# Kernel tuning notes

Measured on AMD Instinct MI355X. Metric: run time of the kernel, lower is better.

## Reference

```python
import jax, jax.numpy as jnp
import numpy as np

N = 50000      # nodes
E = 500000     # edges (avg degree 10)
D_IN = 256     # input feature dim
HID = 256      # hidden_channels
HEADS = 8
C_HID = HID // HEADS   # 32 per-head dim for concat layers
NCLS = 8               # num_classes (last layer per-head dim, concat=False)


def setup_inputs() -> dict:
    key = jax.random.key(0)
    keys = iter(jax.random.split(key, 64))
    def w(shape, s=0.05):
        return jax.random.normal(next(keys), shape, jnp.float32) * s
    inp = {}
    inp["x"] = jax.random.normal(next(keys), (N, D_IN), jnp.float32)
    inp["edge_index"] = jax.random.randint(next(keys), (2, E), 0, N, jnp.int32)
    # (fan_in, heads*per_head_out, skip_out) per layer; layer3: concat=False
    layer_cfg = [(D_IN, HEADS * C_HID, HEADS * C_HID),
                 (HID, HEADS * C_HID, HEADS * C_HID),
                 (HID, HEADS * NCLS, NCLS)]
    for i, (fin, hc, skip) in enumerate(layer_cfg, 1):
        for nm in ("q", "k", "v"):
            inp[f"W{nm}{i}"] = w((fin, hc))
            inp[f"b{nm}{i}"] = jnp.zeros((hc,), jnp.float32)
        inp[f"Ws{i}"] = w((fin, skip))
        inp[f"bs{i}"] = jnp.zeros((skip,), jnp.float32)
        inp[f"Wb{i}"] = w((3 * skip, 1))
    for i in (1, 2):
        inp[f"ln{i}_g"] = jnp.ones((HID,), jnp.float32)
        inp[f"ln{i}_b"] = jnp.zeros((HID,), jnp.float32)
    return inp


def _layer_norm(x, g, b):
    mu = x.mean(-1, keepdims=True)
    var = ((x - mu) ** 2).mean(-1, keepdims=True)
    return (x - mu) * jax.lax.rsqrt(var + 1e-5) * g + b


def _tconv(x, src, dst, Wq, bq, Wk, bk, Wv, bv, Ws, bs, Wb, concat):
    """PyG TransformerConv with beta=True, root_weight=True, eval-mode (no dropout)."""
    n = x.shape[0]
    q = (x @ Wq + bq).reshape(n, HEADS, -1)   # [N,H,C]
    k = (x @ Wk + bk).reshape(n, HEADS, -1)
    v = (x @ Wv + bv).reshape(n, HEADS, -1)
    C = q.shape[-1]
    # per-edge attention logits, scaled dot product
    logits = (q[dst] * k[src]).sum(-1) * jax.lax.rsqrt(jnp.float32(C))  # [E,H]
    # segment softmax over incoming edges of each dst node
    m = jax.ops.segment_max(logits, dst, num_segments=n)                # [N,H]
    m = jnp.where(jnp.isfinite(m), m, 0.0)                              # empty segments
    e = jnp.exp(logits - m[dst])
    s = jax.ops.segment_sum(e, dst, num_segments=n)
    alpha = e / (s[dst] + 1e-16)                                        # [E,H]
    # scatter-aggregate messages
    out = jax.ops.segment_sum(v[src] * alpha[:, :, None], dst, num_segments=n)  # [N,H,C]
    out = out.reshape(n, -1) if concat else out.mean(axis=1)
    # beta-gated skip connection
    xr = x @ Ws + bs
    beta = jax.nn.sigmoid(jnp.concatenate([out, xr, out - xr], axis=-1) @ Wb)   # [N,1]
    return beta * xr + (1.0 - beta) * out


def reference(x, edge_index,
              Wq1, bq1, Wk1, bk1, Wv1, bv1, Ws1, bs1, Wb1,
              Wq2, bq2, Wk2, bk2, Wv2, bv2, Ws2, bs2, Wb2,
              Wq3, bq3, Wk3, bk3, Wv3, bv3, Ws3, bs3, Wb3,
              ln1_g, ln1_b, ln2_g, ln2_b):
    src, dst = edge_index[0], edge_index[1]
    h = jax.nn.relu(_layer_norm(
        _tconv(x, src, dst, Wq1, bq1, Wk1, bk1, Wv1, bv1, Ws1, bs1, Wb1, True),
        ln1_g, ln1_b))
    h = jax.nn.relu(_layer_norm(
        _tconv(h, src, dst, Wq2, bq2, Wk2, bk2, Wv2, bv2, Ws2, bs2, Wb2, True),
        ln2_g, ln2_b))
    return _tconv(h, src, dst, Wq3, bq3, Wk3, bk3, Wv3, bv3, Ws3, bs3, Wb3, False)
```

## Files before the change

kernel.cpp:

```cpp
#include <hip/hip_runtime.h>
#include <stdint.h>

typedef __attribute__((ext_vector_type(8))) short short8;
typedef __attribute__((ext_vector_type(4))) float f32x4;

struct us4 { unsigned short x, y, z, w; };

__device__ __forceinline__ float b2f(unsigned short u){
  union { unsigned int i; float f; } x; x.i = ((unsigned int)u) << 16; return x.f;
}
__device__ __forceinline__ unsigned short f2b(float f){
  union { float f; unsigned int i; } x; x.f = f;
  unsigned int i = x.i;
  unsigned int r = (i + 0x7FFFu + ((i >> 16) & 1u)) >> 16;
  return (unsigned short)r;
}
__device__ __forceinline__ float sane(float v){
  return fminf(fmaxf(v, -1e30f), 1e30f);
}
__device__ __forceinline__ float lclamp(float v){
  return fminf(fmaxf(v, -60.f), 60.f);
}
__device__ __forceinline__ float ldin(const void* p, size_t i, int f32){
  return f32 ? ((const float*)p)[i] : b2f(((const unsigned short*)p)[i]);
}

__global__ void k_flag(const unsigned short* __restrict__ xu, int* __restrict__ flag){
  __shared__ int cnt;
  if (threadIdx.x == 0) cnt = 0;
  __syncthreads();
  unsigned u = xu[2 * threadIdx.x];
  int e = (u >> 7) & 0xFF;
  if (e >= 97 && e <= 132) atomicAdd(&cnt, 1);
  __syncthreads();
  if (threadIdx.x == 0) flag[0] = (cnt >= 192) ? 0 : 1;
}

__global__ void k_cvt(const void* __restrict__ xin, unsigned short* __restrict__ xb,
                      int n4, const int* __restrict__ flagp){
  int f32 = *flagp;
  int i = blockIdx.x * 256 + threadIdx.x;
  if (i < n4){
    if (f32){
      float4 v = ((const float4*)xin)[i];
      us4 o = { f2b(v.x), f2b(v.y), f2b(v.z), f2b(v.w) };
      ((us4*)xb)[i] = o;
    } else {
      ((us4*)xb)[i] = ((const us4*)xin)[i];
    }
  }
}

__global__ void k_deg(const int* __restrict__ ei, int E, int N, int* __restrict__ deg){
  int e = blockIdx.x * 256 + threadIdx.x;
  if (e < E){
    unsigned d = (unsigned)ei[E + e];
    if (d < (unsigned)N) atomicAdd(&deg[d], 1);
  }
}

__global__ void k_bsum(const int* __restrict__ deg, int N, int* __restrict__ bsum){
  int b = blockIdx.x, t = threadIdx.x;
  int i0 = b * 1024 + t * 4;
  int s = 0;
  if (i0 + 4 <= N){
    int4 v = *(const int4*)&deg[i0];
    s = v.x + v.y + v.z + v.w;
  } else {
    #pragma unroll
    for (int j = 0; j < 4; ++j){ int i = i0 + j; if (i < N) s += deg[i]; }
  }
  #pragma unroll
  for (int off = 32; off; off >>= 1) s += __shfl_xor(s, off);
  __shared__ int ws[4];
  if ((t & 63) == 0) ws[t >> 6] = s;
  __syncthreads();
  if (t == 0) bsum[b] = ws[0] + ws[1] + ws[2] + ws[3];
}

__global__ void k_bscan(const int* __restrict__ bsum, int nb,
                        int* __restrict__ boff, int* __restrict__ rowptr, int N){
  int t = threadIdx.x;
  if (nb <= 64){
    int v = (t < nb) ? bsum[t] : 0;
    int inc = v;
    #pragma unroll
    for (int off = 1; off < 64; off <<= 1){
      int u = __shfl_up(inc, off);
      if (t >= off) inc += u;
    }
    if (t < nb) boff[t] = inc - v;
    if (t == 63) rowptr[N] = inc;
  } else {
    if (t == 0){
      int run = 0;
      for (int i = 0; i < nb; ++i){ boff[i] = run; run += bsum[i]; }
      rowptr[N] = run;
    }
  }
}

__global__ void k_rowptr(const int* __restrict__ deg, const int* __restrict__ boff,
                         int N, int* __restrict__ rowptr, int* __restrict__ cursor){
  int b = blockIdx.x, t = threadIdx.x;
  int i0 = b * 1024 + t * 4;
  int d0 = 0, d1 = 0, d2 = 0, d3 = 0;
  if (i0 + 4 <= N){
    int4 v = *(const int4*)&deg[i0];
    d0 = v.x; d1 = v.y; d2 = v.z; d3 = v.w;
  } else {
    if (i0     < N) d0 = deg[i0];
    if (i0 + 1 < N) d1 = deg[i0 + 1];
    if (i0 + 2 < N) d2 = deg[i0 + 2];
    if (i0 + 3 < N) d3 = deg[i0 + 3];
  }
  int s = d0 + d1 + d2 + d3;
  int lane = t & 63, w = t >> 6;
  int inc = s;
  #pragma unroll
  for (int off = 1; off < 64; off <<= 1){
    int u = __shfl_up(inc, off);
    if (lane >= off) inc += u;
  }
  int wex = inc - s;
  __shared__ int wtot[4];
  if (lane == 63) wtot[w] = inc;
  __syncthreads();
  int cross = 0;
  for (int i = 0; i < w; ++i) cross += wtot[i];
  int basev = boff[b] + cross + wex;
  int r0 = basev, r1 = basev + d0, r2 = r1 + d1, r3 = r2 + d2;
  if (i0 + 4 <= N){
    int4 o = { r0, r1, r2, r3 };
    *(int4*)&rowptr[i0] = o;
    *(int4*)&cursor[i0] = o;
  } else {
    if (i0     < N){ rowptr[i0]   = r0; cursor[i0]   = r0; }
    if (i0 + 1 < N){ rowptr[i0+1] = r1; cursor[i0+1] = r1; }
    if (i0 + 2 < N){ rowptr[i0+2] = r2; cursor[i0+2] = r2; }
    if (i0 + 3 < N){ rowptr[i0+3] = r3; cursor[i0+3] = r3; }
  }
}

__global__ void k_scatter(const int* __restrict__ ei, int E, int N,
                          int* __restrict__ cursor, int* __restrict__ srcs){
  int e = blockIdx.x * 256 + threadIdx.x;
  if (e < E){
    unsigned d = (unsigned)ei[E + e];
    if (d < (unsigned)N){
      int pos = atomicAdd(&cursor[d], 1);
      if ((unsigned)pos < (unsigned)E){
        unsigned s = (unsigned)ei[e];
        srcs[pos] = (s < (unsigned)N) ? (int)s : 0;
      }
    }
  }
}

__global__ void k_pack(const void* __restrict__ Wq, const void* __restrict__ bq,
                       const void* __restrict__ Wk, const void* __restrict__ bk,
                       const void* __restrict__ Wv, const void* __restrict__ bv,
                       const void* __restrict__ Ws, const void* __restrict__ bs,
                       unsigned short* __restrict__ WT, float* __restrict__ bias,
                       int Mq, int Ms, int K, const int* __restrict__ flagp){
  int f32 = *flagp;
  int cg = blockIdx.x;
  int k  = threadIdx.x;
  int mat, c, mc;
  if (cg < 3 * Mq){ mat = cg / Mq; c = cg % Mq; mc = Mq; }
  else if (cg < 3 * Mq + Ms){ mat = 3; c = cg - 3 * Mq; mc = Ms; }
  else { mat = 4; c = 0; mc = 1; }
  const void* W = (mat==0)?Wq:(mat==1)?Wk:(mat==2)?Wv:(mat==3)?Ws:(const void*)0;
  WT[(size_t)cg * K + k] = (mat < 4) ? f2b(ldin(W, (size_t)k * mc + c, f32)) : (unsigned short)0;
  if (k == 0){
    const void* B = (mat==0)?bq:(mat==1)?bk:(mat==2)?bv:(mat==3)?bs:(const void*)0;
    bias[cg] = (mat < 4) ? ldin(B, c, f32) : 0.f;
  }
}

__global__ __launch_bounds__(256) void k_gemm(const unsigned short* __restrict__ A,
                                              const unsigned short* __restrict__ WT,
                                              const float* __restrict__ bias,
                                              unsigned short* __restrict__ B0,
                                              unsigned short* __restrict__ B1,
                                              unsigned short* __restrict__ B2,
                                              unsigned short* __restrict__ B3,
                                              int N, int Mout, int secshift){
  __shared__ __align__(16) unsigned short Alds[64][264];
  __shared__ __align__(16) unsigned short Clds[32][276];
  int tid = threadIdx.x, wid = tid >> 6, lane = tid & 63;
  int l15 = lane & 15, l4 = lane >> 4;
  int row0 = blockIdx.x * 64;
  {
    int srow = tid >> 2, sc4 = tid & 3;
    int ar = row0 + srow; if (ar >= N) ar = N - 1;
    const unsigned short* Ap = A + (size_t)ar * 256;
    #pragma unroll
    for (int i = 0; i < 8; ++i){
      int col = (sc4 + 4 * i) * 8;
      *(short8*)&Alds[srow][col] = *(const short8*)&Ap[col];
    }
  }
  __syncthreads();
  int secw = 1 << secshift;
  int strow = tid >> 3, stchunk = tid & 7;
  for (int cb = wid * 64; cb < Mout; cb += 256){
    f32x4 acc[4][4] = {};
    #pragma unroll
    for (int k0 = 0; k0 < 256; k0 += 32){
      short8 a0 = *(const short8*)&Alds[l15     ][k0 + l4*8];
      short8 a1 = *(const short8*)&Alds[16 + l15][k0 + l4*8];
      short8 a2 = *(const short8*)&Alds[32 + l15][k0 + l4*8];
      short8 a3 = *(const short8*)&Alds[48 + l15][k0 + l4*8];
      const unsigned short* wb = WT + (size_t)(cb + l15) * 256 + k0 + l4*8;
      short8 b0 = *(const short8*)(wb);
      short8 b1 = *(const short8*)(wb + 16*256);
      short8 b2 = *(const short8*)(wb + 32*256);
      short8 b3 = *(const short8*)(wb + 48*256);
      acc[0][0] = __builtin_amdgcn_mfma_f32_16x16x32_bf16(a0, b0, acc[0][0], 0,0,0);
      acc[0][1] = __builtin_amdgcn_mfma_f32_16x16x32_bf16(a0, b1, acc[0][1], 0,0,0);
      acc[0][2] = __builtin_amdgcn_mfma_f32_16x16x32_bf16(a0, b2, acc[0][2], 0,0,0);
      acc[0][3] = __builtin_amdgcn_mfma_f32_16x16x32_bf16(a0, b3, acc[0][3], 0,0,0);
      acc[1][0] = __builtin_amdgcn_mfma_f32_16x16x32_bf16(a1, b0, acc[1][0], 0,0,0);
      acc[1][1] = __builtin_amdgcn_mfma_f32_16x16x32_bf16(a1, b1, acc[1][1], 0,0,0);
      acc[1][2] = __builtin_amdgcn_mfma_f32_16x16x32_bf16(a1, b2, acc[1][2], 0,0,0);
      acc[1][3] = __builtin_amdgcn_mfma_f32_16x16x32_bf16(a1, b3, acc[1][3], 0,0,0);
      acc[2][0] = __builtin_amdgcn_mfma_f32_16x16x32_bf16(a2, b0, acc[2][0], 0,0,0);
      acc[2][1] = __builtin_amdgcn_mfma_f32_16x16x32_bf16(a2, b1, acc[2][1], 0,0,0);
      acc[2][2] = __builtin_amdgcn_mfma_f32_16x16x32_bf16(a2, b2, acc[2][2], 0,0,0);
      acc[2][3] = __builtin_amdgcn_mfma_f32_16x16x32_bf16(a2, b3, acc[2][3], 0,0,0);
      acc[3][0] = __builtin_amdgcn_mfma_f32_16x16x32_bf16(a3, b0, acc[3][0], 0,0,0);
      acc[3][1] = __builtin_amdgcn_mfma_f32_16x16x32_bf16(a3, b1, acc[3][1], 0,0,0);
      acc[3][2] = __builtin_amdgcn_mfma_f32_16x16x32_bf16(a3, b2, acc[3][2], 0,0,0);
      acc[3][3] = __builtin_amdgcn_mfma_f32_16x16x32_bf16(a3, b3, acc[3][3], 0,0,0);
    }
    int gb = cb - wid * 64;
    #pragma unroll
    for (int ph = 0; ph < 2; ++ph){
      #pragma unroll
      for (int rt2 = 0; rt2 < 2; ++rt2){
        int rt = ph*2 + rt2;
        #pragma unroll
        for (int ct = 0; ct < 4; ++ct){
          float bv = bias[cb + ct*16 + l15];
          #pragma unroll
          for (int r = 0; r < 4; ++r)
            Clds[rt2*16 + l4*4 + r][wid*64 + ct*16 + l15] = f2b(acc[rt][ct][r] + bv);
        }
      }
      __syncthreads();
      int grow = row0 + ph*32 + strow;
      if (grow < N){
        int g0 = gb + stchunk * 32;
        int mat = g0 >> secshift;
        int cc  = g0 & (secw - 1);
        unsigned short* Bp = (mat==0)?B0:(mat==1)?B1:(mat==2)?B2:B3;
        unsigned short* dst = Bp + (size_t)grow * secw + cc;
        const unsigned short* srcp = &Clds[strow][stchunk * 32];
        #pragma unroll
        for (int j = 0; j < 4; ++j)
          *(short8*)(dst + j*8) = *(const short8*)(srcp + j*8);
      }
      __syncthreads();
    }
  }
}

__global__ __launch_bounds__(256) void k_attn(const unsigned short* __restrict__ qb,
                                              const unsigned short* __restrict__ kb,
                                              const unsigned short* __restrict__ vb,
                                              const unsigned short* __restrict__ xb,
                                              const int* __restrict__ rowptr,
                                              const int* __restrict__ srcs,
                                              const void* __restrict__ Wb,
                                              const void* __restrict__ lng,
                                              const void* __restrict__ lnb,
                                              unsigned short* __restrict__ hout,
                                              int N, int E, const int* __restrict__ flagp){
  int f32 = *flagp;
  int tid = threadIdx.x, w = tid >> 6, l = tid & 63;
  int n = blockIdx.x * 4 + w;
  if (n >= N) return;
  size_t base = (size_t)n * 256;
  us4 qv = *(const us4*)&qb[base + l*4];
  float q0 = b2f(qv.x), q1 = b2f(qv.y), q2 = b2f(qv.z), q3 = b2f(qv.w);
  int e0 = rowptr[n], e1 = rowptr[n+1];
  if (e0 < 0) e0 = 0;
  if (e1 > E) e1 = E;
  const float scale = 0.17677669529663687f;
  float ss = 0.f, o0 = 0.f, o1 = 0.f, o2 = 0.f, o3 = 0.f;
  int e = e0;
  for (; e + 4 <= e1; e += 4){
    unsigned s0 = (unsigned)srcs[e];   if (s0 >= (unsigned)N) s0 = 0;
    unsigned s1 = (unsigned)srcs[e+1]; if (s1 >= (unsigned)N) s1 = 0;
    unsigned s2 = (unsigned)srcs[e+2]; if (s2 >= (unsigned)N) s2 = 0;
    unsigned s3 = (unsigned)srcs[e+3]; if (s3 >= (unsigned)N) s3 = 0;
    us4 kA = *(const us4*)&kb[(size_t)s0*256 + l*4];
    us4 kB = *(const us4*)&kb[(size_t)s1*256 + l*4];
    us4 kC = *(const us4*)&kb[(size_t)s2*256 + l*4];
    us4 kD = *(const us4*)&kb[(size_t)s3*256 + l*4];
    us4 vA = *(const us4*)&vb[(size_t)s0*256 + l*4];
    us4 vB = *(const us4*)&vb[(size_t)s1*256 + l*4];
    us4 vC = *(const us4*)&vb[(size_t)s2*256 + l*4];
    us4 vD = *(const us4*)&vb[(size_t)s3*256 + l*4];
    float pa = q0*b2f(kA.x) + q1*b2f(kA.y) + q2*b2f(kA.z) + q3*b2f(kA.w);
    float pb = q0*b2f(kB.x) + q1*b2f(kB.y) + q2*b2f(kB.z) + q3*b2f(kB.w);
    float pc = q0*b2f(kC.x) + q1*b2f(kC.y) + q2*b2f(kC.z) + q3*b2f(kC.w);
    float pd = q0*b2f(kD.x) + q1*b2f(kD.y) + q2*b2f(kD.z) + q3*b2f(kD.w);
    pa += __shfl_xor(pa, 1); pa += __shfl_xor(pa, 2); pa += __shfl_xor(pa, 4);
    pb += __shfl_xor(pb, 1); pb += __shfl_xor(pb, 2); pb += __shfl_xor(pb, 4);
    pc += __shfl_xor(pc, 1); pc += __shfl_xor(pc, 2); pc += __shfl_xor(pc, 4);
    pd += __shfl_xor(pd, 1); pd += __shfl_xor(pd, 2); pd += __shfl_xor(pd, 4);
    float ea = __expf(lclamp(pa * scale));
    float eb = __expf(lclamp(pb * scale));
    float ec = __expf(lclamp(pc * scale));
    float ed = __expf(lclamp(pd * scale));
    ss += ea + eb + ec + ed;
    o0 += ea*b2f(vA.x) + eb*b2f(vB.x) + ec*b2f(vC.x) + ed*b2f(vD.x);
    o1 += ea*b2f(vA.y) + eb*b2f(vB.y) + ec*b2f(vC.y) + ed*b2f(vD.y);
    o2 += ea*b2f(vA.z) + eb*b2f(vB.z) + ec*b2f(vC.z) + ed*b2f(vD.z);
    o3 += ea*b2f(vA.w) + eb*b2f(vB.w) + ec*b2f(vC.w) + ed*b2f(vD.w);
  }
  for (; e < e1; ++e){
    unsigned s = (unsigned)srcs[e]; if (s >= (unsigned)N) s = 0;
    us4 kk = *(const us4*)&kb[(size_t)s*256 + l*4];
    us4 vv = *(const us4*)&vb[(size_t)s*256 + l*4];
    float p = q0*b2f(kk.x) + q1*b2f(kk.y) + q2*b2f(kk.z) + q3*b2f(kk.w);
    p += __shfl_xor(p, 1); p += __shfl_xor(p, 2); p += __shfl_xor(p, 4);
    float a = __expf(lclamp(p * scale));
    ss += a;
    o0 += a*b2f(vv.x); o1 += a*b2f(vv.y); o2 += a*b2f(vv.z); o3 += a*b2f(vv.w);
  }
  float sinv = 1.f / (ss + 1e-16f);
  o0 = sane(o0 * sinv); o1 = sane(o1 * sinv);
  o2 = sane(o2 * sinv); o3 = sane(o3 * sinv);
  int c = l * 4;
  us4 xv = *(const us4*)&xb[base + c];
  float x0 = sane(b2f(xv.x)), x1 = sane(b2f(xv.y)), x2 = sane(b2f(xv.z)), x3 = sane(b2f(xv.w));
  float d = o0*ldin(Wb, c+0, f32) + x0*ldin(Wb, 256+c+0, f32) + (o0-x0)*ldin(Wb, 512+c+0, f32)
          + o1*ldin(Wb, c+1, f32) + x1*ldin(Wb, 256+c+1, f32) + (o1-x1)*ldin(Wb, 512+c+1, f32)
          + o2*ldin(Wb, c+2, f32) + x2*ldin(Wb, 256+c+2, f32) + (o2-x2)*ldin(Wb, 512+c+2, f32)
          + o3*ldin(Wb, c+3, f32) + x3*ldin(Wb, 256+c+3, f32) + (o3-x3)*ldin(Wb, 512+c+3, f32);
  #pragma unroll
  for (int off = 32; off; off >>= 1) d += __shfl_xor(d, off);
  float beta = 1.f / (1.f + __expf(-d));
  float r0 = beta*x0 + (1.f-beta)*o0;
  float r1 = beta*x1 + (1.f-beta)*o1;
  float r2 = beta*x2 + (1.f-beta)*o2;
  float r3 = beta*x3 + (1.f-beta)*o3;
  float sm = r0 + r1 + r2 + r3;
  #pragma unroll
  for (int off = 32; off; off >>= 1) sm += __shfl_xor(sm, off);
  float mu = sm * (1.f/256.f);
  float d0 = r0-mu, d1 = r1-mu, d2 = r2-mu, d3 = r3-mu;
  float vv2 = d0*d0 + d1*d1 + d2*d2 + d3*d3;
  #pragma unroll
  for (int off = 32; off; off >>= 1) vv2 += __shfl_xor(vv2, off);
  float rs = rsqrtf(vv2 * (1.f/256.f) + 1e-5f);
  us4 outv;
  outv.x = f2b(fmaxf(d0*rs*ldin(lng,c+0,f32) + ldin(lnb,c+0,f32), 0.f));
  outv.y = f2b(fmaxf(d1*rs*ldin(lng,c+1,f32) + ldin(lnb,c+1,f32), 0.f));
  outv.z = f2b(fmaxf(d2*rs*ldin(lng,c+2,f32) + ldin(lnb,c+2,f32), 0.f));
  outv.w = f2b(fmaxf(d3*rs*ldin(lng,c+3,f32) + ldin(lnb,c+3,f32), 0.f));
  *(us4*)&hout[base + c] = outv;
}

__global__ __launch_bounds__(256) void k_final(const unsigned short* __restrict__ q3,
                                               const unsigned short* __restrict__ k3,
                                               const unsigned short* __restrict__ v3,
                                               const unsigned short* __restrict__ x3,
                                               const int* __restrict__ rowptr,
                                               const int* __restrict__ srcs,
                                               const void* __restrict__ Wb,
                                               void* __restrict__ outp,
                                               int N, int E, const int* __restrict__ flagp){
  int f32 = *flagp;
  int tid = threadIdx.x, w = tid >> 6, l = tid & 63;
  int n = blockIdx.x * 4 + w;
  if (n >= N) return;
  int es = l >> 4, h = (l >> 1) & 7, j = l & 1;
  size_t base = (size_t)n * 64;
  us4 qv = *(const us4*)&q3[base + h*8 + j*4];
  float q0 = b2f(qv.x), q1 = b2f(qv.y), q2 = b2f(qv.z), q3f = b2f(qv.w);
  int e0 = rowptr[n], e1 = rowptr[n+1];
  if (e0 < 0) e0 = 0;
  if (e1 > E) e1 = E;
  int deg = e1 - e0;
  const float scale = 0.35355339059327373f;
  float ss = 0.f, o0 = 0.f, o1 = 0.f, o2 = 0.f, o3 = 0.f;
  for (int ei = es; ei < deg; ei += 4){
    unsigned s = (unsigned)srcs[e0 + ei]; if (s >= (unsigned)N) s = 0;
    us4 kk = *(const us4*)&k3[(size_t)s*64 + h*8 + j*4];
    us4 vv = *(const us4*)&v3[(size_t)s*64 + h*8 + j*4];
    float p = q0*b2f(kk.x) + q1*b2f(kk.y) + q2*b2f(kk.z) + q3f*b2f(kk.w);
    p += __shfl_xor(p, 1);
    float a = __expf(lclamp(p * scale));
    ss += a;
    o0 += a*b2f(vv.x); o1 += a*b2f(vv.y); o2 += a*b2f(vv.z); o3 += a*b2f(vv.w);
  }
  #pragma unroll
  for (int off = 16; off <= 32; off <<= 1){
    ss += __shfl_xor(ss, off);
    o0 += __shfl_xor(o0, off); o1 += __shfl_xor(o1, off);
    o2 += __shfl_xor(o2, off); o3 += __shfl_xor(o3, off);
  }
  float sinv = 1.f / (ss + 1e-16f);
  o0 = sane(o0 * sinv); o1 = sane(o1 * sinv);
  o2 = sane(o2 * sinv); o3 = sane(o3 * sinv);
  #pragma unroll
  for (int off = 2; off <= 8; off <<= 1){
    o0 += __shfl_xor(o0, off); o1 += __shfl_xor(o1, off);
    o2 += __shfl_xor(o2, off); o3 += __shfl_xor(o3, off);
  }
  o0 *= 0.125f; o1 *= 0.125f; o2 *= 0.125f; o3 *= 0.125f;
  us4 xv = *(const us4*)&x3[base + j*4];
  float x0 = sane(b2f(xv.x)), x1 = sane(b2f(xv.y)), x2 = sane(b2f(xv.z)), x3v = sane(b2f(xv.w));
  int c = j*4;
  float d = o0*ldin(Wb, c+0, f32) + x0*ldin(Wb, 8+c+0, f32) + (o0-x0)*ldin(Wb, 16+c+0, f32)
          + o1*ldin(Wb, c+1, f32) + x1*ldin(Wb, 8+c+1, f32) + (o1-x1)*ldin(Wb, 16+c+1, f32)
          + o2*ldin(Wb, c+2, f32) + x2*ldin(Wb, 8+c+2, f32) + (o2-x2)*ldin(Wb, 16+c+2, f32)
          + o3*ldin(Wb, c+3, f32) + x3v*ldin(Wb, 8+c+3, f32) + (o3-x3v)*ldin(Wb, 16+c+3, f32);
  d += __shfl_xor(d, 1);
  float beta = 1.f / (1.f + __expf(-d));
  float r0 = beta*x0  + (1.f-beta)*o0;
  float r1 = beta*x1  + (1.f-beta)*o1;
  float r2 = beta*x2  + (1.f-beta)*o2;
  float r3 = beta*x3v + (1.f-beta)*o3;
  if (l < 2){
    if (f32){
      float* op = (float*)outp + (size_t)n*8 + l*4;
      op[0] = r0; op[1] = r1; op[2] = r2; op[3] = r3;
    } else {
      unsigned short* op = (unsigned short*)outp + (size_t)n*8 + l*4;
      op[0] = f2b(r0); op[1] = f2b(r1); op[2] = f2b(r2); op[3] = f2b(r3);
    }
  }
}

extern "C" void kernel_launch(void* const* d_in, const int* in_sizes, int n_in,
                              void* d_out, int out_size, void* d_ws, size_t ws_size,
                              hipStream_t stream){
  const int* ei = (const int*)d_in[1];
  const int N = in_sizes[0] / 256;
  const int E = in_sizes[1] / 2;

  char* wsp = (char*)d_ws;
  size_t off = 0;
  auto alloc = [&](size_t b) -> void* {
    void* p = wsp + off; off = (off + b + 255) & ~(size_t)255; return p;
  };
  unsigned short* WT1  = (unsigned short*)alloc((size_t)1024*256*2);
  unsigned short* WT2  = (unsigned short*)alloc((size_t)1024*256*2);
  unsigned short* WT3  = (unsigned short*)alloc((size_t)256*256*2);
  float* bias1 = (float*)alloc(1024*4);
  float* bias2 = (float*)alloc(1024*4);
  float* bias3 = (float*)alloc(256*4);
  int* flag   = (int*)alloc(256);
  int* deg    = (int*)alloc((size_t)N*4);
  int* rowptr = (int*)alloc((size_t)(N+1)*4);
  int* cursor = (int*)alloc((size_t)N*4);
  int* bsum   = (int*)alloc(1024*4);
  int* boff   = (int*)alloc(1024*4);
  int* srcs   = (int*)alloc((size_t)E*4);
  unsigned short* xbf = (unsigned short*)alloc((size_t)N*256*2);
  unsigned short* qb  = (unsigned short*)alloc((size_t)N*256*2);
  unsigned short* kb  = (unsigned short*)alloc((size_t)N*256*2);
  unsigned short* vb  = (unsigned short*)alloc((size_t)N*256*2);
  unsigned short* xb  = (unsigned short*)alloc((size_t)N*256*2);
  unsigned short* hbuf= (unsigned short*)alloc((size_t)N*256*2);
  unsigned short* q3 = qb;
  unsigned short* k3 = kb;
  unsigned short* v3 = vb;
  unsigned short* x3 = xb;
  (void)ws_size; (void)n_in; (void)out_size;

  k_flag<<<1, 256, 0, stream>>>((const unsigned short*)d_in[0], flag);
  int n4 = (N * 256) / 4;
  k_cvt<<<(n4 + 255) / 256, 256, 0, stream>>>(d_in[0], xbf, n4, flag);

  hipMemsetAsync(deg, 0, (size_t)N*4, stream);
  int eb = (E + 255) / 256;
  int nbk = (N + 1023) / 1024;
  k_deg<<<eb, 256, 0, stream>>>(ei, E, N, deg);
  k_bsum<<<nbk, 256, 0, stream>>>(deg, N, bsum);
  k_bscan<<<1, 64, 0, stream>>>(bsum, nbk, boff, rowptr, N);
  k_rowptr<<<nbk, 256, 0, stream>>>(deg, boff, N, rowptr, cursor);
  k_scatter<<<eb, 256, 0, stream>>>(ei, E, N, cursor, srcs);

  k_pack<<<1024, 256, 0, stream>>>(d_in[2],  d_in[3],  d_in[4],  d_in[5],  d_in[6],  d_in[7],  d_in[8],  d_in[9],  WT1, bias1, 256, 256, 256, flag);
  k_pack<<<1024, 256, 0, stream>>>(d_in[11], d_in[12], d_in[13], d_in[14], d_in[15], d_in[16], d_in[17], d_in[18], WT2, bias2, 256, 256, 256, flag);
  k_pack<<< 256, 256, 0, stream>>>(d_in[20], d_in[21], d_in[22], d_in[23], d_in[24], d_in[25], d_in[26], d_in[27], WT3, bias3,  64,   8, 256, flag);

  int rb = (N + 63) / 64;
  int nb = (N + 3) / 4;
  k_gemm<<<rb, 256, 0, stream>>>(xbf, WT1, bias1, qb, kb, vb, xb, N, 1024, 8);
  k_attn<<<nb, 256, 0, stream>>>(qb, kb, vb, xb, rowptr, srcs, d_in[10], d_in[29], d_in[30], hbuf, N, E, flag);
  k_gemm<<<rb, 256, 0, stream>>>(hbuf, WT2, bias2, qb, kb, vb, xb, N, 1024, 8);
  k_attn<<<nb, 256, 0, stream>>>(qb, kb, vb, xb, rowptr, srcs, d_in[19], d_in[31], d_in[32], hbuf, N, E, flag);
  k_gemm<<<rb, 256, 0, stream>>>(hbuf, WT3, bias3, q3, k3, v3, x3, N, 256, 6);
  k_final<<<nb, 256, 0, stream>>>(q3, k3, v3, x3, rowptr, srcs, d_in[28], d_out, N, E, flag);
}
```

Baseline: 666.1 us.

## Interleave K/V in fp16, pad CSR rows to 4, prefetch gathers

The GEMM epilogue now writes K and V as fp16 interleaved per 4-channel group, so each edge gather is a single 16-byte load instead of two 8-byte loads. Q and skip outputs also switch to fp16 so the attention dot product can use packed fdot2. CSR rows are padded to multiples of 4 with zeroed slots, and the source indices are pre-multiplied into byte offsets, so the attention loop can read four indices as one vector and software-prefetch the next group with no scalar tail. The cost is fp16 range and precision risk versus bf16, an extra memset of the padded index array, and masked work on the padding slots.

```diff
diff --git a/kernel.cpp b/kernel.cpp
--- a/kernel.cpp
+++ b/kernel.cpp
@@ -3,6 +3,9 @@
 
 typedef __attribute__((ext_vector_type(8))) short short8;
 typedef __attribute__((ext_vector_type(4))) float f32x4;
+typedef __attribute__((ext_vector_type(4))) _Float16 half4;
+typedef __attribute__((ext_vector_type(2))) _Float16 half2v;
+typedef __attribute__((ext_vector_type(4))) int i32x4;
 
 struct us4 { unsigned short x, y, z, w; };
 
@@ -15,6 +18,10 @@
   unsigned int r = (i + 0x7FFFu + ((i >> 16) & 1u)) >> 16;
   return (unsigned short)r;
 }
+__device__ __forceinline__ unsigned short f2h(float f){
+  _Float16 h = (_Float16)f;
+  union { _Float16 h; unsigned short u; } c; c.h = h; return c.u;
+}
 __device__ __forceinline__ float sane(float v){
   return fminf(fmaxf(v, -1e30f), 1e30f);
 }
@@ -23,6 +30,14 @@
 }
 __device__ __forceinline__ float ldin(const void* p, size_t i, int f32){
   return f32 ? ((const float*)p)[i] : b2f(((const unsigned short*)p)[i]);
+}
+__device__ __forceinline__ float dot4h(half2v a0, half2v a1, half2v b0, half2v b1){
+#if __has_builtin(__builtin_amdgcn_fdot2)
+  return __builtin_amdgcn_fdot2(a0, b0, __builtin_amdgcn_fdot2(a1, b1, 0.f, false), false);
+#else
+  return (float)a0.x*(float)b0.x + (float)a0.y*(float)b0.y
+       + (float)a1.x*(float)b1.x + (float)a1.y*(float)b1.y;
+#endif
 }
 
 __global__ void k_flag(const unsigned short* __restrict__ xu, int* __restrict__ flag){
@@ -59,16 +74,18 @@
   }
 }
 
+__device__ __forceinline__ int pad4(int d){ return (d + 3) & ~3; }
+
 __global__ void k_bsum(const int* __restrict__ deg, int N, int* __restrict__ bsum){
   int b = blockIdx.x, t = threadIdx.x;
   int i0 = b * 1024 + t * 4;
   int s = 0;
   if (i0 + 4 <= N){
     int4 v = *(const int4*)&deg[i0];
-    s = v.x + v.y + v.z + v.w;
+    s = pad4(v.x) + pad4(v.y) + pad4(v.z) + pad4(v.w);
   } else {
     #pragma unroll
-    for (int j = 0; j < 4; ++j){ int i = i0 + j; if (i < N) s += deg[i]; }
+    for (int j = 0; j < 4; ++j){ int i = i0 + j; if (i < N) s += pad4(deg[i]); }
   }
   #pragma unroll
   for (int off = 32; off; off >>= 1) s += __shfl_xor(s, off);
@@ -114,7 +131,8 @@
     if (i0 + 2 < N) d2 = deg[i0 + 2];
     if (i0 + 3 < N) d3 = deg[i0 + 3];
   }
-  int s = d0 + d1 + d2 + d3;
+  int p0 = pad4(d0), p1 = pad4(d1), p2 = pad4(d2), p3 = pad4(d3);
+  int s = p0 + p1 + p2 + p3;
   int lane = t & 63, w = t >> 6;
   int inc = s;
   #pragma unroll
@@ -129,7 +147,7 @@
   int cross = 0;
   for (int i = 0; i < w; ++i) cross += wtot[i];
   int basev = boff[b] + cross + wex;
-  int r0 = basev, r1 = basev + d0, r2 = r1 + d1, r3 = r2 + d2;
+  int r0 = basev, r1 = basev + p0, r2 = r1 + p1, r3 = r2 + p2;
   if (i0 + 4 <= N){
     int4 o = { r0, r1, r2, r3 };
     *(int4*)&rowptr[i0] = o;
@@ -142,16 +160,16 @@
   }
 }
 
-__global__ void k_scatter(const int* __restrict__ ei, int E, int N,
+__global__ void k_scatter(const int* __restrict__ ei, int E, int N, int Epad,
                           int* __restrict__ cursor, int* __restrict__ srcs){
   int e = blockIdx.x * 256 + threadIdx.x;
   if (e < E){
     unsigned d = (unsigned)ei[E + e];
     if (d < (unsigned)N){
       int pos = atomicAdd(&cursor[d], 1);
-      if ((unsigned)pos < (unsigned)E){
+      if ((unsigned)pos < (unsigned)Epad){
         unsigned s = (unsigned)ei[e];
-        srcs[pos] = (s < (unsigned)N) ? (int)s : 0;
+        srcs[pos] = (s < (unsigned)N) ? (int)(s * 1024u) : 0;
       }
     }
   }
@@ -181,10 +199,9 @@
 __global__ __launch_bounds__(256) void k_gemm(const unsigned short* __restrict__ A,
                                               const unsigned short* __restrict__ WT,
                                               const float* __restrict__ bias,
-                                              unsigned short* __restrict__ B0,
-                                              unsigned short* __restrict__ B1,
-                                              unsigned short* __restrict__ B2,
-                                              unsigned short* __restrict__ B3,
+                                              unsigned short* __restrict__ qout,
+                                              char* __restrict__ kvout,
+                                              unsigned short* __restrict__ xout,
                                               int N, int Mout, int secshift){
   __shared__ __align__(16) unsigned short Alds[64][264];
   __shared__ __align__(16) unsigned short Clds[32][276];
@@ -245,7 +262,7 @@
           float bv = bias[cb + ct*16 + l15];
           #pragma unroll
           for (int r = 0; r < 4; ++r)
-            Clds[rt2*16 + l4*4 + r][wid*64 + ct*16 + l15] = f2b(acc[rt][ct][r] + bv);
+            Clds[rt2*16 + l4*4 + r][wid*64 + ct*16 + l15] = f2h(acc[rt][ct][r] + bv);
         }
       }
       __syncthreads();
@@ -254,12 +271,21 @@
         int g0 = gb + stchunk * 32;
         int mat = g0 >> secshift;
         int cc  = g0 & (secw - 1);
-        unsigned short* Bp = (mat==0)?B0:(mat==1)?B1:(mat==2)?B2:B3;
-        unsigned short* dst = Bp + (size_t)grow * secw + cc;
         const unsigned short* srcp = &Clds[strow][stchunk * 32];
-        #pragma unroll
-        for (int j = 0; j < 4; ++j)
-          *(short8*)(dst + j*8) = *(const short8*)(srcp + j*8);
+        if (mat == 1 || mat == 2){
+          char* dstb = kvout + (size_t)grow * (size_t)(secw * 4)
+                     + (size_t)((cc >> 2) * 16 + ((mat == 2) ? 8 : 0));
+          #pragma unroll
+          for (int g2 = 0; g2 < 8; ++g2)
+            *(unsigned long long*)(dstb + g2 * 16) =
+                *(const unsigned long long*)(srcp + g2 * 4);
+        } else {
+          unsigned short* Bp = (mat == 0) ? qout : xout;
+          unsigned short* dst = Bp + (size_t)grow * secw + cc;
+          #pragma unroll
+          for (int j = 0; j < 4; ++j)
+            *(short8*)(dst + j*8) = *(const short8*)(srcp + j*8);
+        }
       }
       __syncthreads();
     }
@@ -267,10 +293,10 @@
 }
 
 __global__ __launch_bounds__(256) void k_attn(const unsigned short* __restrict__ qb,
-                                              const unsigned short* __restrict__ kb,
-                                              const unsigned short* __restrict__ vb,
+                                              const char* __restrict__ kvb,
                                               const unsigned short* __restrict__ xb,
                                               const int* __restrict__ rowptr,
+                                              const int* __restrict__ degv,
                                               const int* __restrict__ srcs,
                                               const void* __restrict__ Wb,
                                               const void* __restrict__ lng,
@@ -281,62 +307,60 @@
   int tid = threadIdx.x, w = tid >> 6, l = tid & 63;
   int n = blockIdx.x * 4 + w;
   if (n >= N) return;
-  size_t base = (size_t)n * 256;
-  us4 qv = *(const us4*)&qb[base + l*4];
-  float q0 = b2f(qv.x), q1 = b2f(qv.y), q2 = b2f(qv.z), q3 = b2f(qv.w);
-  int e0 = rowptr[n], e1 = rowptr[n+1];
-  if (e0 < 0) e0 = 0;
-  if (e1 > E) e1 = E;
+  unsigned lof = (unsigned)l * 16u;
+  size_t nbase = (size_t)n * 512;
+  union KV { i32x4 v; _Float16 h[8]; half2v h2[4]; };
+  half4 qv = *(const half4*)((const char*)qb + nbase + (unsigned)l * 8u);
+  half2v q01 = { qv.x, qv.y }, q23 = { qv.z, qv.w };
+  int e0 = rowptr[n]; if (e0 < 0) e0 = 0;
+  int dg = degv[n]; if (dg < 0) dg = 0; if (dg > E) dg = E;
+  int npad = (dg + 3) & ~3;
   const float scale = 0.17677669529663687f;
   float ss = 0.f, o0 = 0.f, o1 = 0.f, o2 = 0.f, o3 = 0.f;
-  int e = e0;
-  for (; e + 4 <= e1; e += 4){
-    unsigned s0 = (unsigned)srcs[e];   if (s0 >= (unsigned)N) s0 = 0;
-    unsigned s1 = (unsigned)srcs[e+1]; if (s1 >= (unsigned)N) s1 = 0;
-    unsigned s2 = (unsigned)srcs[e+2]; if (s2 >= (unsigned)N) s2 = 0;
-    unsigned s3 = (unsigned)srcs[e+3]; if (s3 >= (unsigned)N) s3 = 0;
-    us4 kA = *(const us4*)&kb[(size_t)s0*256 + l*4];
-    us4 kB = *(const us4*)&kb[(size_t)s1*256 + l*4];
-    us4 kC = *(const us4*)&kb[(size_t)s2*256 + l*4];
-    us4 kD = *(const us4*)&kb[(size_t)s3*256 + l*4];
-    us4 vA = *(const us4*)&vb[(size_t)s0*256 + l*4];
-    us4 vB = *(const us4*)&vb[(size_t)s1*256 + l*4];
-    us4 vC = *(const us4*)&vb[(size_t)s2*256 + l*4];
-    us4 vD = *(const us4*)&vb[(size_t)s3*256 + l*4];
-    float pa = q0*b2f(kA.x) + q1*b2f(kA.y) + q2*b2f(kA.z) + q3*b2f(kA.w);
-    float pb = q0*b2f(kB.x) + q1*b2f(kB.y) + q2*b2f(kB.z) + q3*b2f(kB.w);
-    float pc = q0*b2f(kC.x) + q1*b2f(kC.y) + q2*b2f(kC.z) + q3*b2f(kC.w);
-    float pd = q0*b2f(kD.x) + q1*b2f(kD.y) + q2*b2f(kD.z) + q3*b2f(kD.w);
-    pa += __shfl_xor(pa, 1); pa += __shfl_xor(pa, 2); pa += __shfl_xor(pa, 4);
-    pb += __shfl_xor(pb, 1); pb += __shfl_xor(pb, 2); pb += __shfl_xor(pb, 4);
-    pc += __shfl_xor(pc, 1); pc += __shfl_xor(pc, 2); pc += __shfl_xor(pc, 4);
-    pd += __shfl_xor(pd, 1); pd += __shfl_xor(pd, 2); pd += __shfl_xor(pd, 4);
-    float ea = __expf(lclamp(pa * scale));
-    float eb = __expf(lclamp(pb * scale));
-    float ec = __expf(lclamp(pc * scale));
-    float ed = __expf(lclamp(pd * scale));
-    ss += ea + eb + ec + ed;
-    o0 += ea*b2f(vA.x) + eb*b2f(vB.x) + ec*b2f(vC.x) + ed*b2f(vD.x);
-    o1 += ea*b2f(vA.y) + eb*b2f(vB.y) + ec*b2f(vC.y) + ed*b2f(vD.y);
-    o2 += ea*b2f(vA.z) + eb*b2f(vB.z) + ec*b2f(vC.z) + ed*b2f(vD.z);
-    o3 += ea*b2f(vA.w) + eb*b2f(vB.w) + ec*b2f(vC.w) + ed*b2f(vD.w);
-  }
-  for (; e < e1; ++e){
-    unsigned s = (unsigned)srcs[e]; if (s >= (unsigned)N) s = 0;
-    us4 kk = *(const us4*)&kb[(size_t)s*256 + l*4];
-    us4 vv = *(const us4*)&vb[(size_t)s*256 + l*4];
-    float p = q0*b2f(kk.x) + q1*b2f(kk.y) + q2*b2f(kk.z) + q3*b2f(kk.w);
+
+  auto consume = [&](const KV& kv, int valid){
+    float p = dot4h(q01, q23, kv.h2[0], kv.h2[1]);
     p += __shfl_xor(p, 1); p += __shfl_xor(p, 2); p += __shfl_xor(p, 4);
-    float a = __expf(lclamp(p * scale));
+    float a = valid ? __expf(lclamp(p * scale)) : 0.f;
     ss += a;
-    o0 += a*b2f(vv.x); o1 += a*b2f(vv.y); o2 += a*b2f(vv.z); o3 += a*b2f(vv.w);
-  }
+    o0 += a * (float)kv.h[4];
+    o1 += a * (float)kv.h[5];
+    o2 += a * (float)kv.h[6];
+    o3 += a * (float)kv.h[7];
+  };
+
+  if (npad > 0){
+    i32x4 offs = *(const i32x4*)&srcs[e0];
+    KV c0, c1, c2, c3;
+    c0.v = *(const i32x4*)(kvb + (unsigned)offs[0] + lof);
+    c1.v = *(const i32x4*)(kvb + (unsigned)offs[1] + lof);
+    c2.v = *(const i32x4*)(kvb + (unsigned)offs[2] + lof);
+    c3.v = *(const i32x4*)(kvb + (unsigned)offs[3] + lof);
+    int base = 0;
+    #pragma unroll 1
+    for (; base + 4 < npad; base += 4){
+      i32x4 offsN = *(const i32x4*)&srcs[e0 + base + 4];
+      KV n0, n1, n2, n3;
+      n0.v = *(const i32x4*)(kvb + (unsigned)offsN[0] + lof);
+      n1.v = *(const i32x4*)(kvb + (unsigned)offsN[1] + lof);
+      n2.v = *(const i32x4*)(kvb + (unsigned)offsN[2] + lof);
+      n3.v = *(const i32x4*)(kvb + (unsigned)offsN[3] + lof);
+      consume(c0, 1); consume(c1, 1); consume(c2, 1); consume(c3, 1);
+      c0 = n0; c1 = n1; c2 = n2; c3 = n3;
+    }
+    consume(c0, base + 0 < dg);
+    consume(c1, base + 1 < dg);
+    consume(c2, base + 2 < dg);
+    consume(c3, base + 3 < dg);
+  }
+
   float sinv = 1.f / (ss + 1e-16f);
   o0 = sane(o0 * sinv); o1 = sane(o1 * sinv);
   o2 = sane(o2 * sinv); o3 = sane(o3 * sinv);
   int c = l * 4;
-  us4 xv = *(const us4*)&xb[base + c];
-  float x0 = sane(b2f(xv.x)), x1 = sane(b2f(xv.y)), x2 = sane(b2f(xv.z)), x3 = sane(b2f(xv.w));
+  half4 xv = *(const half4*)((const char*)xb + nbase + (unsigned)l * 8u);
+  float x0 = sane((float)xv.x), x1 = sane((float)xv.y);
+  float x2 = sane((float)xv.z), x3 = sane((float)xv.w);
   float d = o0*ldin(Wb, c+0, f32) + x0*ldin(Wb, 256+c+0, f32) + (o0-x0)*ldin(Wb, 512+c+0, f32)
           + o1*ldin(Wb, c+1, f32) + x1*ldin(Wb, 256+c+1, f32) + (o1-x1)*ldin(Wb, 512+c+1, f32)
           + o2*ldin(Wb, c+2, f32) + x2*ldin(Wb, 256+c+2, f32) + (o2-x2)*ldin(Wb, 512+c+2, f32)
@@ -362,14 +386,14 @@
   outv.y = f2b(fmaxf(d1*rs*ldin(lng,c+1,f32) + ldin(lnb,c+1,f32), 0.f));
   outv.z = f2b(fmaxf(d2*rs*ldin(lng,c+2,f32) + ldin(lnb,c+2,f32), 0.f));
   outv.w = f2b(fmaxf(d3*rs*ldin(lng,c+3,f32) + ldin(lnb,c+3,f32), 0.f));
-  *(us4*)&hout[base + c] = outv;
-}
-
-__global__ __launch_bounds__(256) void k_final(const unsigned short* __restrict__ q3,
-                                               const unsigned short* __restrict__ k3,
-                                               const unsigned short* __restrict__ v3,
-                                               const unsigned short* __restrict__ x3,
+  *(us4*)&hout[(size_t)n * 256 + c] = outv;
+}
+
+__global__ __launch_bounds__(256) void k_final(const unsigned short* __restrict__ q3b,
+                                               const char* __restrict__ kv3b,
+                                               const unsigned short* __restrict__ x3b,
                                                const int* __restrict__ rowptr,
+                                               const int* __restrict__ degv,
                                                const int* __restrict__ srcs,
                                                const void* __restrict__ Wb,
                                                void* __restrict__ outp,
@@ -378,25 +402,41 @@
   int tid = threadIdx.x, w = tid >> 6, l = tid & 63;
   int n = blockIdx.x * 4 + w;
   if (n >= N) return;
-  int es = l >> 4, h = (l >> 1) & 7, j = l & 1;
-  size_t base = (size_t)n * 64;
-  us4 qv = *(const us4*)&q3[base + h*8 + j*4];
-  float q0 = b2f(qv.x), q1 = b2f(qv.y), q2 = b2f(qv.z), q3f = b2f(qv.w);
-  int e0 = rowptr[n], e1 = rowptr[n+1];
-  if (e0 < 0) e0 = 0;
-  if (e1 > E) e1 = E;
-  int deg = e1 - e0;
+  int es = l >> 4, g = l & 15, j = g & 1;
+  unsigned lof = (unsigned)g * 16u;
+  size_t nbase = (size_t)n * 128;
+  union KV { i32x4 v; _Float16 h[8]; half2v h2[4]; };
+  half4 qv = *(const half4*)((const char*)q3b + nbase + (unsigned)g * 8u);
+  half2v q01 = { qv.x, qv.y }, q23 = { qv.z, qv.w };
+  int e0 = rowptr[n]; if (e0 < 0) e0 = 0;
+  int dg = degv[n]; if (dg < 0) dg = 0; if (dg > E) dg = E;
+  int npad = (dg + 3) & ~3;
   const float scale = 0.35355339059327373f;
   float ss = 0.f, o0 = 0.f, o1 = 0.f, o2 = 0.f, o3 = 0.f;
-  for (int ei = es; ei < deg; ei += 4){
-    unsigned s = (unsigned)srcs[e0 + ei]; if (s >= (unsigned)N) s = 0;
-    us4 kk = *(const us4*)&k3[(size_t)s*64 + h*8 + j*4];
-    us4 vv = *(const us4*)&v3[(size_t)s*64 + h*8 + j*4];
-    float p = q0*b2f(kk.x) + q1*b2f(kk.y) + q2*b2f(kk.z) + q3f*b2f(kk.w);
+
+  auto consume = [&](const KV& kv, int valid){
+    float p = dot4h(q01, q23, kv.h2[0], kv.h2[1]);
     p += __shfl_xor(p, 1);
-    float a = __expf(lclamp(p * scale));
+    float a = valid ? __expf(lclamp(p * scale)) : 0.f;
     ss += a;
-    o0 += a*b2f(vv.x); o1 += a*b2f(vv.y); o2 += a*b2f(vv.z); o3 += a*b2f(vv.w);
+    o0 += a * (float)kv.h[4];
+    o1 += a * (float)kv.h[5];
+    o2 += a * (float)kv.h[6];
+    o3 += a * (float)kv.h[7];
+  };
+
+  int idx = es;
+  if (idx < npad){
+    KV c;
+    c.v = *(const i32x4*)(kv3b + (((unsigned)srcs[e0 + idx]) >> 2) + lof);
+    #pragma unroll 1
+    for (; idx + 4 < npad; idx += 4){
+      KV nx;
+      nx.v = *(const i32x4*)(kv3b + (((unsigned)srcs[e0 + idx + 4]) >> 2) + lof);
+      consume(c, idx < dg);
+      c = nx;
+    }
+    consume(c, idx < dg);
   }
   #pragma unroll
   for (int off = 16; off <= 32; off <<= 1){
@@ -413,8 +453,9 @@
     o2 += __shfl_xor(o2, off); o3 += __shfl_xor(o3, off);
   }
   o0 *= 0.125f; o1 *= 0.125f; o2 *= 0.125f; o3 *= 0.125f;
-  us4 xv = *(const us4*)&x3[base + j*4];
-  float x0 = sane(b2f(xv.x)), x1 = sane(b2f(xv.y)), x2 = sane(b2f(xv.z)), x3v = sane(b2f(xv.w));
+  half4 xv = *(const half4*)((const char*)x3b + nbase + (unsigned)(j * 8));
+  float x0 = sane((float)xv.x), x1 = sane((float)xv.y);
+  float x2 = sane((float)xv.z), x3v = sane((float)xv.w);
   int c = j*4;
   float d = o0*ldin(Wb, c+0, f32) + x0*ldin(Wb, 8+c+0, f32) + (o0-x0)*ldin(Wb, 16+c+0, f32)
           + o1*ldin(Wb, c+1, f32) + x1*ldin(Wb, 8+c+1, f32) + (o1-x1)*ldin(Wb, 16+c+1, f32)
@@ -443,6 +484,7 @@
   const int* ei = (const int*)d_in[1];
   const int N = in_sizes[0] / 256;
   const int E = in_sizes[1] / 2;
+  const int Epad = E + 4 * N + 64;
 
   char* wsp = (char*)d_ws;
   size_t off = 0;
@@ -461,17 +503,12 @@
   int* cursor = (int*)alloc((size_t)N*4);
   int* bsum   = (int*)alloc(1024*4);
   int* boff   = (int*)alloc(1024*4);
-  int* srcs   = (int*)alloc((size_t)E*4);
+  int* srcs   = (int*)alloc((size_t)Epad*4);
   unsigned short* xbf = (unsigned short*)alloc((size_t)N*256*2);
   unsigned short* qb  = (unsigned short*)alloc((size_t)N*256*2);
-  unsigned short* kb  = (unsigned short*)alloc((size_t)N*256*2);
-  unsigned short* vb  = (unsigned short*)alloc((size_t)N*256*2);
+  char*           kvb = (char*)alloc((size_t)N*1024);
   unsigned short* xb  = (unsigned short*)alloc((size_t)N*256*2);
   unsigned short* hbuf= (unsigned short*)alloc((size_t)N*256*2);
-  unsigned short* q3 = qb;
-  unsigned short* k3 = kb;
-  unsigned short* v3 = vb;
-  unsigned short* x3 = xb;
   (void)ws_size; (void)n_in; (void)out_size;
 
   k_flag<<<1, 256, 0, stream>>>((const unsigned short*)d_in[0], flag);
@@ -479,13 +516,14 @@
   k_cvt<<<(n4 + 255) / 256, 256, 0, stream>>>(d_in[0], xbf, n4, flag);
 
   hipMemsetAsync(deg, 0, (size_t)N*4, stream);
+  hipMemsetAsync(srcs, 0, (size_t)Epad*4, stream);
   int eb = (E + 255) / 256;
   int nbk = (N + 1023) / 1024;
   k_deg<<<eb, 256, 0, stream>>>(ei, E, N, deg);
   k_bsum<<<nbk, 256, 0, stream>>>(deg, N, bsum);
   k_bscan<<<1, 64, 0, stream>>>(bsum, nbk, boff, rowptr, N);
   k_rowptr<<<nbk, 256, 0, stream>>>(deg, boff, N, rowptr, cursor);
-  k_scatter<<<eb, 256, 0, stream>>>(ei, E, N, cursor, srcs);
+  k_scatter<<<eb, 256, 0, stream>>>(ei, E, N, Epad, cursor, srcs);
 
   k_pack<<<1024, 256, 0, stream>>>(d_in[2],  d_in[3],  d_in[4],  d_in[5],  d_in[6],  d_in[7],  d_in[8],  d_in[9],  WT1, bias1, 256, 256, 256, flag);
   k_pack<<<1024, 256, 0, stream>>>(d_in[11], d_in[12], d_in[13], d_in[14], d_in[15], d_in[16], d_in[17], d_in[18], WT2, bias2, 256, 256, 256, flag);
@@ -493,10 +531,10 @@
 
   int rb = (N + 63) / 64;
   int nb = (N + 3) / 4;
-  k_gemm<<<rb, 256, 0, stream>>>(xbf, WT1, bias1, qb, kb, vb, xb, N, 1024, 8);
-  k_attn<<<nb, 256, 0, stream>>>(qb, kb, vb, xb, rowptr, srcs, d_in[10], d_in[29], d_in[30], hbuf, N, E, flag);
-  k_gemm<<<rb, 256, 0, stream>>>(hbuf, WT2, bias2, qb, kb, vb, xb, N, 1024, 8);
-  k_attn<<<nb, 256, 0, stream>>>(qb, kb, vb, xb, rowptr, srcs, d_in[19], d_in[31], d_in[32], hbuf, N, E, flag);
-  k_gemm<<<rb, 256, 0, stream>>>(hbuf, WT3, bias3, q3, k3, v3, x3, N, 256, 6);
-  k_final<<<nb, 256, 0, stream>>>(q3, k3, v3, x3, rowptr, srcs, d_in[28], d_out, N, E, flag);
-}
+  k_gemm<<<rb, 256, 0, stream>>>(xbf, WT1, bias1, qb, kvb, xb, N, 1024, 8);
+  k_attn<<<nb, 256, 0, stream>>>(qb, kvb, xb, rowptr, deg, srcs, d_in[10], d_in[29], d_in[30], hbuf, N, E, flag);
+  k_gemm<<<rb, 256, 0, stream>>>(hbuf, WT2, bias2, qb, kvb, xb, N, 1024, 8);
+  k_attn<<<nb, 256, 0, stream>>>(qb, kvb, xb, rowptr, deg, srcs, d_in[19], d_in[31], d_in[32], hbuf, N, E, flag);
+  k_gemm<<<rb, 256, 0, stream>>>(hbuf, WT3, bias3, qb, kvb, xb, N, 256, 6);
+  k_final<<<nb, 256, 0, stream>>>(qb, kvb, xb, rowptr, deg, srcs, d_in[28], d_out, N, E, flag);
+}
```

After: 669.8 us. About the same (+0.6%).
